# Performance work log

Hardware: AMD Instinct MI355X
Metric: run time of the kernel (lower is better)

The kernel has to match this reference:

```python
import jax, jax.numpy as jnp
import numpy as np

H, W = 14, 14
MIN_RATIO, MAX_RATIO = 0.25, 1.0
GLOBAL_RATIO = 0.5


def setup_inputs() -> dict:
    key = jax.random.key(0)
    motion = jax.random.uniform(key, (512, 1, 224, 224), dtype=jnp.float32)
    return {"motion_magnitude": motion, "num_tokens": 6272}


def reference(motion_magnitude, num_tokens):
    B, C, Hin, Win = motion_magnitude.shape
    # adaptive_avg_pool2d to (14,14): input dims are exact multiples -> block mean
    fh, fw = Hin // H, Win // W
    motion_resized = motion_magnitude.reshape(B, C, H, fh, W, fw).mean(axis=(3, 5))  # (B,1,H,W)
    m_min = motion_resized.min()
    m_max = motion_resized.max()
    motion_normalized = (motion_resized - m_min) / (m_max - m_min + 1e-6)
    importance_scores = motion_normalized[:, 0]  # (B,H,W)
    compression_ratio = MIN_RATIO + (MAX_RATIO - MIN_RATIO) * importance_scores
    current_avg = compression_ratio.mean()
    scale = GLOBAL_RATIO / (current_avg + 1e-6)
    scaled = jnp.clip(compression_ratio * scale, MIN_RATIO, MAX_RATIO)
    compression_ratio = jnp.where(current_avg > 0, scaled, compression_ratio)

    # --- vectorized get_merge_indices (replaces double Python loop) ---
    ratio_flat = compression_ratio.reshape(B, H * W)
    tpp = num_tokens // (H * W)  # tokens per patch
    k = jnp.clip(jnp.round(ratio_flat * tpp).astype(jnp.int32), 1, tpp)  # (B,HW)
    # keep first k tokens inside each patch's contiguous block of tpp tokens
    within = jnp.arange(tpp, dtype=jnp.int32)  # (tpp,)
    mask = (within[None, None, :] < k[:, :, None]).astype(jnp.float32)  # (B,HW,tpp)
    merge_mask = mask.reshape(B, H * W * tpp)
    if H * W * tpp < num_tokens:  # pad remainder with zeros (kept at 0 in original)
        merge_mask = jnp.pad(merge_mask, ((0, 0), (0, num_tokens - H * W * tpp)))
    return compression_ratio, importance_scores, merge_mask
```

## Files before the change

### kernel.cpp

```cpp
#include <hip/hip_runtime.h>
#include <math.h>

#define HW2   196
#define IMG   224
#define IMG2  (224*224)
#define SPB   4

__global__ __launch_bounds__(256) void k_patch_mean(const float* __restrict__ in,
                                                    float* __restrict__ resized,
                                                    float* __restrict__ pmin,
                                                    float* __restrict__ pmax,
                                                    double* __restrict__ psum,
                                                    int nstrips) {
    const int t    = threadIdx.x;
    const int wid  = t >> 6;
    const int lane = t & 63;
    const int s    = blockIdx.x * SPB + wid;

    float4 acc = make_float4(0.f, 0.f, 0.f, 0.f);
    if (s < nstrips && lane < 56) {
        const float4* strip = (const float4*)(in + (size_t)s * (16 * IMG)) + lane;
        #pragma unroll
        for (int r = 0; r < 16; ++r) {
            float4 v = strip[r * 56];
            acc.x += v.x; acc.y += v.y; acc.z += v.z; acc.w += v.w;
        }
    }
    float h = (acc.x + acc.y) + (acc.z + acc.w);
    h += __shfl_xor(h, 1, 64);
    h += __shfl_xor(h, 2, 64);
    float g = __shfl(h, lane * 4, 64);

    float  mnv = INFINITY, mxv = -INFINITY;
    double sv  = 0.0;
    if (s < nstrips && lane < 14) {
        float mean = g * (1.0f / 256.0f);
        resized[s * 14 + lane] = mean;
        mnv = mean; mxv = mean; sv = (double)mean;
    }
    #pragma unroll
    for (int off = 32; off; off >>= 1) {
        mnv = fminf(mnv, __shfl_xor(mnv, off, 64));
        mxv = fmaxf(mxv, __shfl_xor(mxv, off, 64));
        sv += __shfl_xor(sv, off, 64);
    }
    __shared__ float  smn[SPB], smx[SPB];
    __shared__ double ssm[SPB];
    if (lane == 0) { smn[wid] = mnv; smx[wid] = mxv; ssm[wid] = sv; }
    __syncthreads();
    if (t == 0) {
        pmin[blockIdx.x] = fminf(fminf(smn[0], smn[1]), fminf(smn[2], smn[3]));
        pmax[blockIdx.x] = fmaxf(fmaxf(smx[0], smx[1]), fmaxf(smx[2], smx[3]));
        psum[blockIdx.x] = ssm[0] + ssm[1] + ssm[2] + ssm[3];
    }
}

__global__ __launch_bounds__(256) void k_output(const float* __restrict__ resized,
                                                const float* __restrict__ pmin,
                                                const float* __restrict__ pmax,
                                                const double* __restrict__ psum,
                                                int nblk1,
                                                float* __restrict__ out,
                                                int npair, int tpp, int num_tokens) {
    int t = threadIdx.x;
    float  mn = INFINITY, mx = -INFINITY;
    double s  = 0.0;
    for (int i = t; i < nblk1; i += 256) {
        mn = fminf(mn, pmin[i]);
        mx = fmaxf(mx, pmax[i]);
        s += psum[i];
    }
    #pragma unroll
    for (int off = 32; off; off >>= 1) {
        mn = fminf(mn, __shfl_xor(mn, off, 64));
        mx = fmaxf(mx, __shfl_xor(mx, off, 64));
        s += __shfl_xor(s, off, 64);
    }
    __shared__ float  smn[4], smx[4];
    __shared__ double ssm[4];
    __shared__ float  sc3[3];
    int wid = t >> 6, lane = t & 63;
    if (lane == 0) { smn[wid] = mn; smx[wid] = mx; ssm[wid] = s; }
    __syncthreads();
    if (t == 0) {
        mn = fminf(fminf(smn[0], smn[1]), fminf(smn[2], smn[3]));
        mx = fmaxf(fmaxf(smx[0], smx[1]), fmaxf(smx[2], smx[3]));
        s  = ssm[0] + ssm[1] + ssm[2] + ssm[3];
        float denom = __fadd_rn(__fsub_rn(mx, mn), 1e-6f);
        double mean     = s / (double)npair;
        double avg_norm = (mean - (double)mn) / (double)denom;
        double cur_avg  = 0.25 + 0.75 * avg_norm;
        sc3[0] = mn;
        sc3[1] = denom;
        sc3[2] = (float)(0.5 / (cur_avg + 1e-6));
    }
    __syncthreads();
    const float fmn = sc3[0], fden = sc3[1], fscale = sc3[2];

    int base = blockIdx.x * 256;
    int g = base + t;
    __shared__ int      kk[256];
    __shared__ unsigned kbase[256];
    int k = 0;
    unsigned kb = 0;
    if (g < npair) {
        float r = resized[g];
        float norm   = __fdiv_rn(__fsub_rn(r, fmn), fden);
        float ratio0 = __fadd_rn(0.25f, __fmul_rn(0.75f, norm));
        float sc     = __fmul_rn(ratio0, fscale);
        float ratio  = fminf(fmaxf(sc, 0.25f), 1.0f);
        k = (int)rintf(__fmul_rn(ratio, (float)tpp));
        k = min(max(k, 1), tpp);
        out[g]         = ratio;
        out[npair + g] = norm;
        unsigned b = (unsigned)g / HW2;
        unsigned p = (unsigned)g - b * HW2;
        kb = b * (unsigned)num_tokens + p * (unsigned)tpp;
    }
    kk[t]    = k;
    kbase[t] = kb;
    __syncthreads();

    float* mask = out + 2 * (size_t)npair;
    int nprs = min(256, npair - base);
    if ((tpp & 3) == 0) {
        int tq = tpp >> 2;
        int total4 = nprs * tq;
        for (int i = t; i < total4; i += 256) {
            int pr = (unsigned)i / (unsigned)tq;
            int wi = (i - pr * tq) * 4;
            int kv = kk[pr];
            float4 m;
            m.x = (wi     < kv) ? 1.0f : 0.0f;
            m.y = (wi + 1 < kv) ? 1.0f : 0.0f;
            m.z = (wi + 2 < kv) ? 1.0f : 0.0f;
            m.w = (wi + 3 < kv) ? 1.0f : 0.0f;
            *(float4*)(mask + (size_t)kbase[pr] + wi) = m;
        }
    } else {
        int total = nprs * tpp;
        for (int i = t; i < total; i += 256) {
            int pr = (unsigned)i / (unsigned)tpp;
            int wi = i - pr * tpp;
            mask[(size_t)kbase[pr] + wi] = (wi < kk[pr]) ? 1.0f : 0.0f;
        }
    }
}

__global__ void k_pad(float* __restrict__ mask, int B, int num_tokens, int used) {
    int per = num_tokens - used;
    int idx = blockIdx.x * 256 + threadIdx.x;
    int tot = B * per;
    if (idx < tot) {
        int b = idx / per;
        int j = idx - b * per;
        mask[(size_t)b * num_tokens + used + j] = 0.0f;
    }
}

extern "C" void kernel_launch(void* const* d_in, const int* in_sizes, int n_in,
                              void* d_out, int out_size, void* d_ws, size_t ws_size,
                              hipStream_t stream) {
    const float* motion = (const float*)d_in[0];
    int nelem = in_sizes[0];
    int B     = nelem / IMG2;
    int npair = B * HW2;
    int num_tokens = (out_size - 2 * npair) / B;
    int tpp   = num_tokens / HW2;

    int nstrips = npair / 14;
    int nb1 = (nstrips + SPB - 1) / SPB;

    float* resized = (float*)d_ws;
    size_t off = ((size_t)npair * sizeof(float) + 7) & ~(size_t)7;
    double* psum = (double*)((char*)d_ws + off);
    float*  pmin = (float*)(psum + nb1);
    float*  pmax = pmin + nb1;

    hipLaunchKernelGGL(k_patch_mean, dim3(nb1), dim3(256), 0, stream,
                       motion, resized, pmin, pmax, psum, nstrips);

    int nb2 = (npair + 255) / 256;
    hipLaunchKernelGGL(k_output, dim3(nb2), dim3(256), 0, stream,
                       resized, pmin, pmax, psum, nb1,
                       (float*)d_out, npair, tpp, num_tokens);

    int used = HW2 * tpp;
    if (used < num_tokens) {
        int tot = B * (num_tokens - used);
        hipLaunchKernelGGL(k_pad, dim3((tot + 255) / 256), dim3(256), 0, stream,
                           (float*)d_out + 2 * (size_t)npair, B, num_tokens, used);
    }
}
```

Before: 28.49 us.

## Split global scalar reduction into single-block kernel and use nontemporal loads

Moves the global min/max/sum reduction out of every k_output block into a dedicated single-block k_scalars kernel, so output blocks only read three precomputed scalars. The per-block partial reduction in k_patch_mean now gathers the block's means in shared memory and reduces them in one wave using float partial sums instead of double. Input loads use nontemporal builtin vector loads to avoid polluting cache. This adds an extra kernel launch and slightly changes summation precision.

```diff
diff --git a/kernel.cpp b/kernel.cpp
--- a/kernel.cpp
+++ b/kernel.cpp
@@ -6,24 +6,26 @@
 #define IMG2  (224*224)
 #define SPB   4
 
+typedef float f32x4 __attribute__((ext_vector_type(4)));
+
 __global__ __launch_bounds__(256) void k_patch_mean(const float* __restrict__ in,
                                                     float* __restrict__ resized,
                                                     float* __restrict__ pmin,
                                                     float* __restrict__ pmax,
-                                                    double* __restrict__ psum,
+                                                    float* __restrict__ psum,
                                                     int nstrips) {
     const int t    = threadIdx.x;
     const int wid  = t >> 6;
     const int lane = t & 63;
     const int s    = blockIdx.x * SPB + wid;
 
-    float4 acc = make_float4(0.f, 0.f, 0.f, 0.f);
+    f32x4 acc = (f32x4)(0.f);
     if (s < nstrips && lane < 56) {
-        const float4* strip = (const float4*)(in + (size_t)s * (16 * IMG)) + lane;
+        const f32x4* strip = (const f32x4*)(in + (size_t)s * (16 * IMG)) + lane;
         #pragma unroll
         for (int r = 0; r < 16; ++r) {
-            float4 v = strip[r * 56];
-            acc.x += v.x; acc.y += v.y; acc.z += v.z; acc.w += v.w;
+            f32x4 v = __builtin_nontemporal_load(&strip[r * 56]);
+            acc += v;
         }
     }
     float h = (acc.x + acc.y) + (acc.z + acc.w);
@@ -31,44 +33,49 @@
     h += __shfl_xor(h, 2, 64);
     float g = __shfl(h, lane * 4, 64);
 
-    float  mnv = INFINITY, mxv = -INFINITY;
-    double sv  = 0.0;
+    __shared__ float means[SPB * 14];
     if (s < nstrips && lane < 14) {
         float mean = g * (1.0f / 256.0f);
         resized[s * 14 + lane] = mean;
-        mnv = mean; mxv = mean; sv = (double)mean;
-    }
-    #pragma unroll
-    for (int off = 32; off; off >>= 1) {
-        mnv = fminf(mnv, __shfl_xor(mnv, off, 64));
-        mxv = fmaxf(mxv, __shfl_xor(mxv, off, 64));
-        sv += __shfl_xor(sv, off, 64);
-    }
-    __shared__ float  smn[SPB], smx[SPB];
-    __shared__ double ssm[SPB];
-    if (lane == 0) { smn[wid] = mnv; smx[wid] = mxv; ssm[wid] = sv; }
+        means[wid * 14 + lane] = mean;
+    }
     __syncthreads();
-    if (t == 0) {
-        pmin[blockIdx.x] = fminf(fminf(smn[0], smn[1]), fminf(smn[2], smn[3]));
-        pmax[blockIdx.x] = fmaxf(fmaxf(smx[0], smx[1]), fmaxf(smx[2], smx[3]));
-        psum[blockIdx.x] = ssm[0] + ssm[1] + ssm[2] + ssm[3];
-    }
-}
-
-__global__ __launch_bounds__(256) void k_output(const float* __restrict__ resized,
-                                                const float* __restrict__ pmin,
-                                                const float* __restrict__ pmax,
-                                                const double* __restrict__ psum,
-                                                int nblk1,
-                                                float* __restrict__ out,
-                                                int npair, int tpp, int num_tokens) {
+
+    if (wid == 0) {
+        float mnv = INFINITY, mxv = -INFINITY, sv = 0.0f;
+        if (lane < SPB * 14) {
+            int s2 = blockIdx.x * SPB + (lane / 14);
+            if (s2 < nstrips) {
+                float m = means[lane];
+                mnv = m; mxv = m; sv = m;
+            }
+        }
+        #pragma unroll
+        for (int off = 32; off; off >>= 1) {
+            mnv = fminf(mnv, __shfl_xor(mnv, off, 64));
+            mxv = fmaxf(mxv, __shfl_xor(mxv, off, 64));
+            sv += __shfl_xor(sv, off, 64);
+        }
+        if (lane == 0) {
+            pmin[blockIdx.x] = mnv;
+            pmax[blockIdx.x] = mxv;
+            psum[blockIdx.x] = sv;
+        }
+    }
+}
+
+__global__ __launch_bounds__(256) void k_scalars(const float* __restrict__ pmin,
+                                                 const float* __restrict__ pmax,
+                                                 const float* __restrict__ psum,
+                                                 int nblk1, int npair,
+                                                 float* __restrict__ sc3) {
     int t = threadIdx.x;
     float  mn = INFINITY, mx = -INFINITY;
     double s  = 0.0;
     for (int i = t; i < nblk1; i += 256) {
         mn = fminf(mn, pmin[i]);
         mx = fmaxf(mx, pmax[i]);
-        s += psum[i];
+        s += (double)psum[i];
     }
     #pragma unroll
     for (int off = 32; off; off >>= 1) {
@@ -78,7 +85,6 @@
     }
     __shared__ float  smn[4], smx[4];
     __shared__ double ssm[4];
-    __shared__ float  sc3[3];
     int wid = t >> 6, lane = t & 63;
     if (lane == 0) { smn[wid] = mn; smx[wid] = mx; ssm[wid] = s; }
     __syncthreads();
@@ -94,7 +100,13 @@
         sc3[1] = denom;
         sc3[2] = (float)(0.5 / (cur_avg + 1e-6));
     }
-    __syncthreads();
+}
+
+__global__ __launch_bounds__(256) void k_output(const float* __restrict__ resized,
+                                                const float* __restrict__ sc3,
+                                                float* __restrict__ out,
+                                                int npair, int tpp, int num_tokens) {
+    int t = threadIdx.x;
     const float fmn = sc3[0], fden = sc3[1], fscale = sc3[2];
 
     int base = blockIdx.x * 256;
@@ -172,18 +184,20 @@
     int nb1 = (nstrips + SPB - 1) / SPB;
 
     float* resized = (float*)d_ws;
-    size_t off = ((size_t)npair * sizeof(float) + 7) & ~(size_t)7;
-    double* psum = (double*)((char*)d_ws + off);
-    float*  pmin = (float*)(psum + nb1);
-    float*  pmax = pmin + nb1;
+    float* psum = resized + npair;
+    float* pmin = psum + nb1;
+    float* pmax = pmin + nb1;
+    float* sc3  = pmax + nb1;
 
     hipLaunchKernelGGL(k_patch_mean, dim3(nb1), dim3(256), 0, stream,
                        motion, resized, pmin, pmax, psum, nstrips);
 
+    hipLaunchKernelGGL(k_scalars, dim3(1), dim3(256), 0, stream,
+                       pmin, pmax, psum, nb1, npair, sc3);
+
     int nb2 = (npair + 255) / 256;
     hipLaunchKernelGGL(k_output, dim3(nb2), dim3(256), 0, stream,
-                       resized, pmin, pmax, psum, nb1,
-                       (float*)d_out, npair, tpp, num_tokens);
+                       resized, sc3, (float*)d_out, npair, tpp, num_tokens);
 
     int used = HW2 * tpp;
     if (used < num_tokens) {
```

Result: no change. 28.22 us (-1.0%).
